# Kernel optimization log

Hardware: AMD Instinct MI355X
Metric: run time of the kernel (lower is better)

The kernel has to match this reference:

```python
import jax, jax.numpy as jnp
import numpy as np

N = 50000
E = 800000
IN_DIM, HID, OUT, DW = 128, 96, 40, 64
N_LBL = 10


def _deg_inv_sqrt(dst, n):
    # PyG gcn_norm: degree over target nodes of (A + I)
    deg = jax.ops.segment_sum(jnp.ones((dst.shape[0],), jnp.float32), dst, num_segments=n) + 1.0
    return jnp.where(deg > 0, 1.0 / jnp.sqrt(deg), 0.0)


def gcn_conv(h_in, W, b, src, dst, dinv):
    # GCNConv: out = D^-1/2 (A + I) D^-1/2 (X W) + b
    h = h_in @ W                                  # [N, F]
    norm = (dinv[src] * dinv[dst])[:, None]       # [E, 1]
    agg = jax.ops.segment_sum(h[src] * norm, dst, num_segments=h.shape[0])
    agg = agg + h * (dinv * dinv)[:, None]        # self-loop term
    return agg + b


def setup_inputs() -> dict:
    key = jax.random.key(0)
    ks = jax.random.split(key, 12)
    inp = {
        "x": jax.random.normal(ks[0], (N, IN_DIM), jnp.float32),
        "y": jax.random.uniform(ks[1], (N, OUT), jnp.float32),
        "edge_index": jax.random.randint(ks[2], (2, E), 0, N, jnp.int64 if jax.config.read("jax_enable_x64") else jnp.int32),
        "deep_walk_emb": jax.random.normal(ks[3], (N, DW), jnp.float32),
        # learned params
        "W_gcn1": jax.random.normal(ks[4], (IN_DIM, HID), jnp.float32) * (1.0 / np.sqrt(IN_DIM)),
        "b_gcn1": jnp.zeros((HID,), jnp.float32),
        "W_gcn2": jax.random.normal(ks[5], (HID, HID), jnp.float32) * (1.0 / np.sqrt(HID)),
        "b_gcn2": jnp.zeros((HID,), jnp.float32),
        "W_lbl": jax.random.normal(ks[6], (N_LBL, OUT, OUT), jnp.float32) * (1.0 / np.sqrt(OUT)),
        "b_lbl": jnp.zeros((N_LBL, OUT), jnp.float32),
        "W_fuse": jax.random.normal(ks[7], (HID + OUT + DW, OUT), jnp.float32) * (1.0 / np.sqrt(HID + OUT + DW)),
        "b_fuse": jnp.zeros((OUT,), jnp.float32),
    }
    return inp


def reference(x, y, edge_index, deep_walk_emb,
              W_gcn1, b_gcn1, W_gcn2, b_gcn2,
              W_lbl, b_lbl, W_fuse, b_fuse):
    src, dst = edge_index[0], edge_index[1]
    dinv = _deg_inv_sqrt(dst, x.shape[0])

    # feature propagation: 2 stacked GCNConv layers
    h = gcn_conv(x, W_gcn1, b_gcn1, src, dst, dinv)
    h = gcn_conv(h, W_gcn2, b_gcn2, src, dst, dinv)

    # label propagation: 10 stacked GCNConv layers via scan over stacked weights
    def step(carry, wb):
        W, b = wb
        return gcn_conv(carry, W, b, src, dst, dinv), None

    x_label, _ = jax.lax.scan(step, y, (W_lbl, b_lbl))

    fused = jnp.concatenate([h, x_label, deep_walk_emb], axis=1)  # [N, HID+OUT+DW]
    out = fused @ W_fuse + b_fuse
    return jax.nn.sigmoid(out)
```

## Files before the change

### kernel.cpp

```cpp
#include <hip/hip_runtime.h>
#include <hip/hip_bf16.h>
#include <math.h>

#define THREADS 256
typedef _Float16 h16;

__device__ __forceinline__ void ld8h(const h16* p, float* f) {
    union { uint4 u; h16 h[8]; } c;
    c.u = *(const uint4*)p;
#pragma unroll
    for (int j = 0; j < 8; ++j) f[j] = (float)c.h[j];
}

__global__ void count_kernel(const int* __restrict__ dst, int* __restrict__ cnt, int E) {
    int e = blockIdx.x * blockDim.x + threadIdx.x;
    if (e < E) atomicAdd(&cnt[dst[e]], 1);
}

__global__ __launch_bounds__(256) void scanp1_pre_kernel(
    const int* __restrict__ cnt, int* __restrict__ partial, int n, int NB,
    const float* __restrict__ Wl, const float* __restrict__ bl,
    const float* __restrict__ W1, const float* __restrict__ W2,
    const float* __restrict__ b1,
    float* __restrict__ C0, float* __restrict__ betas,
    float* __restrict__ W12, float* __restrict__ betaf1)
{
    __shared__ __align__(16) float smem[9216];
    const int tid = threadIdx.x;
    const int bid = blockIdx.x;

    if (bid < NB) {
        int* red = (int*)smem;
        int base = bid * 1024 + tid * 4;
        int s = 0;
        if (base + 3 < n) {
            int4 v = *(const int4*)(cnt + base);
            s = v.x + v.y + v.z + v.w;
        } else {
            for (int k = 0; k < 4; k++) { int i = base + k; if (i < n) s += cnt[i]; }
        }
        red[tid] = s;
        __syncthreads();
        for (int off = 128; off > 0; off >>= 1) {
            if (tid < off) red[tid] += red[tid + off];
            __syncthreads();
        }
        if (tid == 0) partial[bid] = red[0];
        return;
    }

    if (bid == NB) {
        float* Ca  = smem;
        float* Cb  = smem + 1600;
        float* sWm = smem + 3200;
        float* bls = smem + 4800;
        for (int idx = tid; idx < 100; idx += 256)
            ((float4*)bls)[idx] = ((const float4*)bl)[idx];
        for (int idx = tid; idx < 1600; idx += 256)
            Ca[idx] = ((idx / 40) == (idx % 40)) ? 1.f : 0.f;
        if (tid < 40) betas[9 * 40 + tid] = bl[9 * 40 + tid];
        __syncthreads();
        float* cur = Ca;
        float* nxt = Cb;
        for (int m = 9; m >= 0; --m) {
            for (int idx = tid; idx < 400; idx += 256)
                ((float4*)sWm)[idx] = ((const float4*)(Wl + (size_t)m * 1600))[idx];
            __syncthreads();
            for (int sid = tid; sid < 400; sid += 256) {
                int i = sid / 10, jq = sid - (sid / 10) * 10;
                const float* wr = &sWm[i * 40];
                const float4* c4 = (const float4*)cur;
                float4 a = make_float4(0.f, 0.f, 0.f, 0.f);
#pragma unroll
                for (int k = 0; k < 40; ++k) {
                    float w = wr[k];
                    float4 c = c4[k * 10 + jq];
                    a.x = fmaf(w, c.x, a.x); a.y = fmaf(w, c.y, a.y);
                    a.z = fmaf(w, c.z, a.z); a.w = fmaf(w, c.w, a.w);
                }
                ((float4*)nxt)[sid] = a;
            }
            __syncthreads();
            if (m >= 1 && tid < 40) {
                float s = 0.f;
                const float* br = &bls[(m - 1) * 40];
#pragma unroll
                for (int k = 0; k < 40; ++k) s = fmaf(br[k], nxt[k * 40 + tid], s);
                betas[(size_t)(m - 1) * 40 + tid] = s;
            }
            float* t = cur; cur = nxt; nxt = t;
            __syncthreads();
        }
        for (int idx = tid; idx < 1600; idx += 256) C0[idx] = cur[idx];
        return;
    }

    float* sW2 = smem;
    for (int idx = tid; idx < 2304; idx += 256)
        ((float4*)sW2)[idx] = ((const float4*)W2)[idx];
    __syncthreads();
    int idx = (bid - NB - 1) * 256 + tid;
    {
        int i = idx / 96, j = idx - (idx / 96) * 96;
        float s = 0.f;
        const float* wr = W1 + (size_t)i * 96;
#pragma unroll 8
        for (int k = 0; k < 96; ++k) s = fmaf(wr[k], sW2[k * 96 + j], s);
        W12[idx] = s;
    }
    if (bid == NB + 1 && tid < 96) {
        float s = 0.f;
        for (int k = 0; k < 96; ++k) s = fmaf(b1[k], sW2[k * 96 + tid], s);
        betaf1[tid] = s;
    }
}

__global__ __launch_bounds__(256) void scan_p2(int* __restrict__ partial, int* __restrict__ rowptr, int nb, int n) {
    __shared__ int sm[256];
    int tid = threadIdx.x;
    int v = (tid < nb) ? partial[tid] : 0;
    sm[tid] = v;
    __syncthreads();
    int acc = v;
    for (int off = 1; off < 256; off <<= 1) {
        int t = (tid >= off) ? sm[tid - off] : 0;
        __syncthreads();
        acc += t;
        sm[tid] = acc;
        __syncthreads();
    }
    if (tid < nb) partial[tid] = acc - v;
    if (tid == 255) rowptr[n] = sm[255];
}

__global__ __launch_bounds__(256) void scan_p3(const int* __restrict__ cnt, const int* __restrict__ partial,
                                               int* __restrict__ rowptr, int* __restrict__ cursor,
                                               float* __restrict__ dinv, int n) {
    __shared__ int tsum[256];
    int tid = threadIdx.x;
    int base = blockIdx.x * 1024 + tid * 4;
    int v0 = 0, v1 = 0, v2 = 0, v3 = 0;
    if (base + 3 < n) {
        int4 t = *(const int4*)(cnt + base);
        v0 = t.x; v1 = t.y; v2 = t.z; v3 = t.w;
    } else {
        if (base + 0 < n) v0 = cnt[base + 0];
        if (base + 1 < n) v1 = cnt[base + 1];
        if (base + 2 < n) v2 = cnt[base + 2];
        if (base + 3 < n) v3 = cnt[base + 3];
    }
    int s = v0 + v1 + v2 + v3;
    tsum[tid] = s;
    __syncthreads();
    int acc = s;
    for (int off = 1; off < 256; off <<= 1) {
        int t = (tid >= off) ? tsum[tid - off] : 0;
        __syncthreads();
        acc += t;
        tsum[tid] = acc;
        __syncthreads();
    }
    int run = partial[blockIdx.x] + acc - s;
    int vv[4] = {v0, v1, v2, v3};
    for (int k = 0; k < 4; k++) {
        int i = base + k;
        if (i < n) {
            rowptr[i] = run; cursor[i] = run; run += vv[k];
            dinv[i] = rsqrtf((float)vv[k] + 1.0f);
        }
    }
}

template<int FIN, int FOUT, typename TX>
__device__ __forceinline__ void gemm_body(
    const TX* __restrict__ X, const float* __restrict__ W,
    const float* __restrict__ dinv, h16* __restrict__ Y, int n,
    float* sX, float* sW, int bid, int tid)
{
    constexpr int KC = (FIN % 32 == 0) ? 32 : FIN;
    constexpr int NCHUNK = FIN / KC;
    constexpr int TN = (FOUT + 15) / 16;
    constexpr int BM = 64;
    constexpr int KP = KC + 4;

    const int tj = tid & 15;
    const int ti = tid >> 4;
    const int i0 = bid * BM;

    float acc[4][TN] = {};

    for (int c = 0; c < NCHUNK; ++c) {
        const int k0 = c * KC;
        __syncthreads();
        if constexpr (sizeof(TX) == 2) {
            constexpr int K8 = KC / 8;
            for (int v = tid; v < BM * K8; v += 256) {
                int r = v / K8, q = v - r * K8;
                int gi = i0 + r;
                float f[8] = {0.f, 0.f, 0.f, 0.f, 0.f, 0.f, 0.f, 0.f};
                if (gi < n) ld8h((const h16*)X + (size_t)gi * FIN + k0 + q * 8, f);
                float* p = &sX[r * KP + q * 8];
#pragma unroll
                for (int j = 0; j < 8; ++j) p[j] = f[j];
            }
        } else {
            constexpr int K4 = KC / 4;
            for (int v = tid; v < BM * K4; v += 256) {
                int r = v / K4, q = v - r * K4;
                int gi = i0 + r;
                float4 val = (gi < n) ? *(const float4*)((const float*)X + (size_t)gi * FIN + k0 + q * 4)
                                      : make_float4(0.f, 0.f, 0.f, 0.f);
                float* p = &sX[r * KP + q * 4];
                p[0] = val.x; p[1] = val.y; p[2] = val.z; p[3] = val.w;
            }
        }
        for (int v = tid; v < KC * FOUT; v += 256) {
            int kk = v / FOUT;
            int j = v - kk * FOUT;
            sW[j * KP + kk] = W[(size_t)(k0 + kk) * FOUT + j];
        }
        __syncthreads();
#pragma unroll
        for (int kk = 0; kk < KC; kk += 4) {
            float4 xv[4];
#pragma unroll
            for (int m = 0; m < 4; ++m)
                xv[m] = *(const float4*)&sX[(ti + 16 * m) * KP + kk];
#pragma unroll
            for (int u = 0; u < TN; ++u) {
                float4 wv = *(const float4*)&sW[(tj + 16 * u) * KP + kk];
#pragma unroll
                for (int m = 0; m < 4; ++m) {
                    acc[m][u] = fmaf(xv[m].x, wv.x, acc[m][u]);
                    acc[m][u] = fmaf(xv[m].y, wv.y, acc[m][u]);
                    acc[m][u] = fmaf(xv[m].z, wv.z, acc[m][u]);
                    acc[m][u] = fmaf(xv[m].w, wv.w, acc[m][u]);
                }
            }
        }
    }

#pragma unroll
    for (int m = 0; m < 4; ++m) {
        int gi = i0 + ti + 16 * m;
        if (gi >= n) continue;
        float dv = dinv[gi];
#pragma unroll
        for (int u = 0; u < TN; ++u) {
            int j = tj + 16 * u;
            if (j < FOUT) Y[(size_t)gi * FOUT + j] = (h16)(acc[m][u] * dv);
        }
    }
}

template<int FIN, int FOUT, typename TX>
__global__ __launch_bounds__(256) void gemm_kernel(
    const TX* __restrict__ X, const float* __restrict__ W,
    const float* __restrict__ dinv, h16* __restrict__ Y, int n)
{
    constexpr int KC = (FIN % 32 == 0) ? 32 : FIN;
    constexpr int KP = KC + 4;
    constexpr int TN = (FOUT + 15) / 16;
    __shared__ __align__(16) float smem[64 * KP + TN * 16 * KP];
    gemm_body<FIN, FOUT, TX>(X, W, dinv, Y, n, smem, smem + 64 * KP, blockIdx.x, threadIdx.x);
}

__global__ __launch_bounds__(256) void scatter_gemm96_kernel(
    const int* __restrict__ src, const int* __restrict__ dst,
    int* __restrict__ cursor, int* __restrict__ col, int E, int gbE,
    const float* __restrict__ x, const float* __restrict__ W12,
    const float* __restrict__ dinv, h16* __restrict__ A96, int n)
{
    __shared__ __align__(16) float smem[64 * 36 + 96 * 36];
    if (blockIdx.x < gbE) {
        int e = blockIdx.x * 256 + threadIdx.x;
        if (e < E) {
            int d = dst[e];
            int p = atomicAdd(&cursor[d], 1);
            col[p] = src[e];
        }
        return;
    }
    gemm_body<128, 96, float>(x, W12, dinv, A96, n, smem, smem + 64 * 36,
                              blockIdx.x - gbE, threadIdx.x);
}

template<int F, int PRE>
__device__ __forceinline__ void agg_body(
    const h16* __restrict__ hs, const int* __restrict__ rowptr,
    const int* __restrict__ col, const float* __restrict__ dinv,
    const float* __restrict__ bias, h16* __restrict__ out, int n,
    int bid, int tid)
{
    constexpr int F8 = F / 8;
    int gt = bid * 256 + tid;
    if (gt >= n * F8) return;
    int i = gt / F8;
    int f = gt - i * F8;
    int s = rowptr[i], e = rowptr[i + 1];
    const h16* base = hs + (size_t)f * 8;
    float acc[8];
    ld8h(hs + (size_t)i * F + f * 8, acc);
    int k = s;
    for (; k + 8 <= e; k += 8) {
        int c[8];
        union { uint4 u; h16 h[8]; } a[8];
#pragma unroll
        for (int q = 0; q < 8; ++q) c[q] = col[k + q];
#pragma unroll
        for (int q = 0; q < 8; ++q) a[q].u = *(const uint4*)(base + (size_t)c[q] * F);
#pragma unroll
        for (int j = 0; j < 8; ++j) {
            float t0 = ((float)a[0].h[j] + (float)a[1].h[j]) + ((float)a[2].h[j] + (float)a[3].h[j]);
            float t1 = ((float)a[4].h[j] + (float)a[5].h[j]) + ((float)a[6].h[j] + (float)a[7].h[j]);
            acc[j] += t0 + t1;
        }
    }
    for (; k + 4 <= e; k += 4) {
        int c0 = col[k], c1 = col[k + 1], c2 = col[k + 2], c3 = col[k + 3];
        union { uint4 u; h16 h[8]; } a0, a1, a2, a3;
        a0.u = *(const uint4*)(base + (size_t)c0 * F);
        a1.u = *(const uint4*)(base + (size_t)c1 * F);
        a2.u = *(const uint4*)(base + (size_t)c2 * F);
        a3.u = *(const uint4*)(base + (size_t)c3 * F);
#pragma unroll
        for (int j = 0; j < 8; ++j)
            acc[j] += ((float)a0.h[j] + (float)a1.h[j]) + ((float)a2.h[j] + (float)a3.h[j]);
    }
    for (; k < e; k++) {
        float v[8];
        ld8h(base + (size_t)col[k] * F, v);
#pragma unroll
        for (int j = 0; j < 8; ++j) acc[j] += v[j];
    }
    float dv = dinv[i];
    float sc = PRE ? dv : 1.f;
    union { uint4 u; h16 h[8]; } o;
#pragma unroll
    for (int j = 0; j < 8; ++j) o.h[j] = (h16)((acc[j] * dv + bias[f * 8 + j]) * sc);
    *(uint4*)(out + (size_t)i * F + f * 8) = o.u;
}

template<int F, int PRE>
__global__ __launch_bounds__(256) void agg_h(
    const h16* __restrict__ hs, const int* __restrict__ rowptr,
    const int* __restrict__ col, const float* __restrict__ dinv,
    const float* __restrict__ bias, h16* __restrict__ out, int n) {
    agg_body<F, PRE>(hs, rowptr, col, dinv, bias, out, n, blockIdx.x, threadIdx.x);
}

template<int PRE2>
__global__ __launch_bounds__(256) void agg_dual_kernel(
    const h16* __restrict__ hsA, const float* __restrict__ biasA, h16* __restrict__ outA,
    const h16* __restrict__ hsB, const float* __restrict__ biasB, h16* __restrict__ outB,
    const int* __restrict__ rowptr, const int* __restrict__ col,
    const float* __restrict__ dinv, int n, int nblkA)
{
    if (blockIdx.x < nblkA)
        agg_body<40, 1>(hsA, rowptr, col, dinv, biasA, outA, n, blockIdx.x, threadIdx.x);
    else
        agg_body<96, PRE2>(hsB, rowptr, col, dinv, biasB, outB, n, blockIdx.x - nblkA, threadIdx.x);
}

template<int KC, typename T>
__device__ __forceinline__ void fuse_chunk(
    const T* __restrict__ src, int FIN, int k0, int wrow0,
    const float* __restrict__ Wf, float* sX, float* sW,
    float acc[4][3], int i0, int n, int tid)
{
    constexpr int KP = 44;
    __syncthreads();
    if constexpr (sizeof(T) == 2) {
        constexpr int K8 = KC / 8;
        for (int v = tid; v < 64 * K8; v += 256) {
            int r = v / K8, q = v - r * K8;
            int gi = i0 + r;
            float f[8] = {0.f, 0.f, 0.f, 0.f, 0.f, 0.f, 0.f, 0.f};
            if (gi < n) ld8h((const h16*)src + (size_t)gi * FIN + k0 + q * 8, f);
            float* p = &sX[r * KP + q * 8];
#pragma unroll
            for (int j = 0; j < 8; ++j) p[j] = f[j];
        }
    } else {
        constexpr int K4 = KC / 4;
        for (int v = tid; v < 64 * K4; v += 256) {
            int r = v / K4, q = v - r * K4;
            int gi = i0 + r;
            float4 val = (gi < n) ? *(const float4*)((const float*)src + (size_t)gi * FIN + k0 + q * 4)
                                  : make_float4(0.f, 0.f, 0.f, 0.f);
            float* p = &sX[r * KP + q * 4];
            p[0] = val.x; p[1] = val.y; p[2] = val.z; p[3] = val.w;
        }
    }
    for (int v = tid; v < KC * 40; v += 256) {
        int kk = v / 40, j = v - kk * 40;
        sW[j * KP + kk] = Wf[(size_t)(wrow0 + kk) * 40 + j];
    }
    __syncthreads();
    int tj = tid & 15, ti = tid >> 4;
#pragma unroll
    for (int kk = 0; kk < KC; kk += 4) {
        float4 xv[4];
#pragma unroll
        for (int m = 0; m < 4; ++m)
            xv[m] = *(const float4*)&sX[(ti + 16 * m) * KP + kk];
#pragma unroll
        for (int u = 0; u < 3; ++u) {
            float4 wv = *(const float4*)&sW[(tj + 16 * u) * KP + kk];
#pragma unroll
            for (int m = 0; m < 4; ++m) {
                acc[m][u] = fmaf(xv[m].x, wv.x, acc[m][u]);
                acc[m][u] = fmaf(xv[m].y, wv.y, acc[m][u]);
                acc[m][u] = fmaf(xv[m].z, wv.z, acc[m][u]);
                acc[m][u] = fmaf(xv[m].w, wv.w, acc[m][u]);
            }
        }
    }
}

__global__ __launch_bounds__(256) void fuse_gemm_kernel(
    const h16* __restrict__ h2, const h16* __restrict__ xl,
    const float* __restrict__ dw, const float* __restrict__ Wf,
    const float* __restrict__ bf, float* __restrict__ out, int n)
{
    __shared__ __align__(16) float sX[64 * 44];
    __shared__ __align__(16) float sW[48 * 44];
    float acc[4][3] = {};
    const int tid = threadIdx.x;
    const int i0 = blockIdx.x * 64;
    fuse_chunk<32>(h2, 96, 0,  0,   Wf, sX, sW, acc, i0, n, tid);
    fuse_chunk<32>(h2, 96, 32, 32,  Wf, sX, sW, acc, i0, n, tid);
    fuse_chunk<32>(h2, 96, 64, 64,  Wf, sX, sW, acc, i0, n, tid);
    fuse_chunk<40>(xl, 40, 0,  96,  Wf, sX, sW, acc, i0, n, tid);
    fuse_chunk<32>(dw, 64, 0,  136, Wf, sX, sW, acc, i0, n, tid);
    fuse_chunk<32>(dw, 64, 32, 168, Wf, sX, sW, acc, i0, n, tid);
    const int tj = tid & 15, ti = tid >> 4;
#pragma unroll
    for (int m = 0; m < 4; ++m) {
        int gi = i0 + ti + 16 * m;
        if (gi >= n) continue;
#pragma unroll
        for (int u = 0; u < 3; ++u) {
            int j = tj + 16 * u;
            if (j < 40) {
                float t = acc[m][u] + bf[j];
                out[(size_t)gi * 40 + j] = 1.f / (1.f + expf(-t));
            }
        }
    }
}

extern "C" void kernel_launch(void* const* d_in, const int* in_sizes, int n_in,
                              void* d_out, int out_size, void* d_ws, size_t ws_size,
                              hipStream_t stream) {
    const float* x   = (const float*)d_in[0];
    const float* y   = (const float*)d_in[1];
    const int*   ei  = (const int*)d_in[2];
    const float* dwe = (const float*)d_in[3];
    const float* W1  = (const float*)d_in[4];
    const float* b1  = (const float*)d_in[5];
    const float* W2  = (const float*)d_in[6];
    const float* b2  = (const float*)d_in[7];
    const float* Wl  = (const float*)d_in[8];
    const float* bl  = (const float*)d_in[9];
    const float* Wf  = (const float*)d_in[10];
    const float* bf  = (const float*)d_in[11];
    float* out = (float*)d_out;

    const int n = in_sizes[0] / 128;
    const int E = in_sizes[2] / 2;
    const int* srcp = ei;
    const int* dstp = ei + E;

    char* ws = (char*)d_ws;
    size_t off = 0;
    auto alloc = [&](size_t bytes) -> void* {
        void* p = ws + off;
        off += bytes;
        off = (off + 255) & ~(size_t)255;
        return p;
    };

    int*   cnt     = (int*)alloc((size_t)n * 4);
    float* dinv    = (float*)alloc((size_t)n * 4);
    int*   rowptr  = (int*)alloc((size_t)(n + 1) * 4);
    int*   cursor  = (int*)alloc((size_t)n * 4);
    int*   partial = (int*)alloc(256 * 4);
    int*   col     = (int*)alloc((size_t)E * 4);
    h16*   A96     = (h16*)alloc((size_t)n * 96 * 2);
    h16*   B96     = (h16*)alloc((size_t)n * 96 * 2);
    h16*   Z0      = (h16*)alloc((size_t)n * 40 * 2);
    h16*   LA      = (h16*)alloc((size_t)n * 40 * 2);
    h16*   LB      = (h16*)alloc((size_t)n * 40 * 2);
    float* C0      = (float*)alloc(1600 * 4);
    float* betas   = (float*)alloc(10 * 40 * 4);
    float* W12     = (float*)alloc(128 * 96 * 4);
    float* betaf1  = (float*)alloc(96 * 4);
    (void)ws_size;

    const int gb_e    = (E + THREADS - 1) / THREADS;
    const int NB      = (n + 1023) / 1024;
    const int gb_gm   = (n + 63) / 64;
    const int gb_a96  = (n * 12 + THREADS - 1) / THREADS;
    const int gb_a40  = (n * 5 + THREADS - 1) / THREADS;

    hipMemsetAsync(cnt, 0, (size_t)n * 4, stream);
    count_kernel<<<gb_e, THREADS, 0, stream>>>(dstp, cnt, E);
    scanp1_pre_kernel<<<NB + 49, THREADS, 0, stream>>>(
        cnt, partial, n, NB, Wl, bl, W1, W2, b1, C0, betas, W12, betaf1);
    scan_p2<<<1, THREADS, 0, stream>>>(partial, rowptr, NB, n);
    scan_p3<<<NB, THREADS, 0, stream>>>(cnt, partial, rowptr, cursor, dinv, n);

    gemm_kernel<40, 40, float><<<gb_gm, THREADS, 0, stream>>>(y, C0, dinv, Z0, n);

    scatter_gemm96_kernel<<<gb_e + gb_gm, THREADS, 0, stream>>>(
        srcp, dstp, cursor, col, E, gb_e, x, W12, dinv, A96, n);

    agg_dual_kernel<1><<<gb_a40 + gb_a96, THREADS, 0, stream>>>(
        Z0, betas + 0, LA, A96, betaf1, B96, rowptr, col, dinv, n, gb_a40);
    agg_dual_kernel<0><<<gb_a40 + gb_a96, THREADS, 0, stream>>>(
        LA, betas + 40, LB, B96, b2, A96, rowptr, col, dinv, n, gb_a40);

    const h16* cur = LB;
    const h16* xl = LB;
    for (int m = 3; m <= 10; m++) {
        h16* nxt = (m & 1) ? LA : LB;
        if (m < 10)
            agg_h<40, 1><<<gb_a40, THREADS, 0, stream>>>(cur, rowptr, col, dinv, betas + (size_t)(m - 1) * 40, nxt, n);
        else
            agg_h<40, 0><<<gb_a40, THREADS, 0, stream>>>(cur, rowptr, col, dinv, betas + (size_t)(m - 1) * 40, nxt, n);
        cur = nxt;
        xl = nxt;
    }

    fuse_gemm_kernel<<<gb_gm, THREADS, 0, stream>>>(A96, xl, dwe, Wf, bf, out, n);
}
```

Measured before the change: 397.2 us.

## Partition edge counting and CSR scatter by destination range across block classes

Replaces the one-thread-per-edge count and scatter kernels with grid-strided kernels in which each of 8 block classes handles only the destinations in its slice of the node range. Each block therefore issues atomics to a narrower region of memory, which is meant to improve atomic locality in L2. The scatter is also split off from the fused scatter+GEMM kernel into its own launch, and the 128→96 GEMM now runs as a separate kernel. In exchange, every block class reads the full dst array (eight passes over the edges), and an extra kernel launch is added.

```diff
diff --git a/kernel.cpp b/kernel.cpp
--- a/kernel.cpp
+++ b/kernel.cpp
@@ -12,9 +12,38 @@
     for (int j = 0; j < 8; ++j) f[j] = (float)c.h[j];
 }
 
-__global__ void count_kernel(const int* __restrict__ dst, int* __restrict__ cnt, int E) {
-    int e = blockIdx.x * blockDim.x + threadIdx.x;
-    if (e < E) atomicAdd(&cnt[dst[e]], 1);
+__global__ __launch_bounds__(256) void count_part_kernel(
+    const int* __restrict__ dst, int* __restrict__ cnt, int E, int n)
+{
+    const int cls = blockIdx.x & 7;
+    const int nb  = gridDim.x >> 3;
+    const int sub = blockIdx.x >> 3;
+    const int lo = (int)((long long)n * cls / 8);
+    const int hi = (int)((long long)n * (cls + 1) / 8);
+    const int stride = nb * 256;
+    for (int e = sub * 256 + threadIdx.x; e < E; e += stride) {
+        int d = dst[e];
+        if (d >= lo && d < hi) atomicAdd(&cnt[d], 1);
+    }
+}
+
+__global__ __launch_bounds__(256) void scatter_part_kernel(
+    const int* __restrict__ src, const int* __restrict__ dst,
+    int* __restrict__ cursor, int* __restrict__ col, int E, int n)
+{
+    const int cls = blockIdx.x & 7;
+    const int nb  = gridDim.x >> 3;
+    const int sub = blockIdx.x >> 3;
+    const int lo = (int)((long long)n * cls / 8);
+    const int hi = (int)((long long)n * (cls + 1) / 8);
+    const int stride = nb * 256;
+    for (int e = sub * 256 + threadIdx.x; e < E; e += stride) {
+        int d = dst[e];
+        if (d >= lo && d < hi) {
+            int p = atomicAdd(&cursor[d], 1);
+            col[p] = src[e];
+        }
+    }
 }
 
 __global__ __launch_bounds__(256) void scanp1_pre_kernel(
@@ -263,26 +292,6 @@
     constexpr int TN = (FOUT + 15) / 16;
     __shared__ __align__(16) float smem[64 * KP + TN * 16 * KP];
     gemm_body<FIN, FOUT, TX>(X, W, dinv, Y, n, smem, smem + 64 * KP, blockIdx.x, threadIdx.x);
-}
-
-__global__ __launch_bounds__(256) void scatter_gemm96_kernel(
-    const int* __restrict__ src, const int* __restrict__ dst,
-    int* __restrict__ cursor, int* __restrict__ col, int E, int gbE,
-    const float* __restrict__ x, const float* __restrict__ W12,
-    const float* __restrict__ dinv, h16* __restrict__ A96, int n)
-{
-    __shared__ __align__(16) float smem[64 * 36 + 96 * 36];
-    if (blockIdx.x < gbE) {
-        int e = blockIdx.x * 256 + threadIdx.x;
-        if (e < E) {
-            int d = dst[e];
-            int p = atomicAdd(&cursor[d], 1);
-            col[p] = src[e];
-        }
-        return;
-    }
-    gemm_body<128, 96, float>(x, W12, dinv, A96, n, smem, smem + 64 * 36,
-                              blockIdx.x - gbE, threadIdx.x);
 }
 
 template<int F, int PRE>
@@ -498,23 +507,22 @@
     float* betaf1  = (float*)alloc(96 * 4);
     (void)ws_size;
 
-    const int gb_e    = (E + THREADS - 1) / THREADS;
     const int NB      = (n + 1023) / 1024;
     const int gb_gm   = (n + 63) / 64;
     const int gb_a96  = (n * 12 + THREADS - 1) / THREADS;
     const int gb_a40  = (n * 5 + THREADS - 1) / THREADS;
+    const int PART_BLOCKS = 2048;
 
     hipMemsetAsync(cnt, 0, (size_t)n * 4, stream);
-    count_kernel<<<gb_e, THREADS, 0, stream>>>(dstp, cnt, E);
+    count_part_kernel<<<PART_BLOCKS, THREADS, 0, stream>>>(dstp, cnt, E, n);
     scanp1_pre_kernel<<<NB + 49, THREADS, 0, stream>>>(
         cnt, partial, n, NB, Wl, bl, W1, W2, b1, C0, betas, W12, betaf1);
     scan_p2<<<1, THREADS, 0, stream>>>(partial, rowptr, NB, n);
     scan_p3<<<NB, THREADS, 0, stream>>>(cnt, partial, rowptr, cursor, dinv, n);
+    scatter_part_kernel<<<PART_BLOCKS, THREADS, 0, stream>>>(srcp, dstp, cursor, col, E, n);
 
     gemm_kernel<40, 40, float><<<gb_gm, THREADS, 0, stream>>>(y, C0, dinv, Z0, n);
-
-    scatter_gemm96_kernel<<<gb_e + gb_gm, THREADS, 0, stream>>>(
-        srcp, dstp, cursor, col, E, gb_e, x, W12, dinv, A96, n);
+    gemm_kernel<128, 96, float><<<gb_gm, THREADS, 0, stream>>>(x, W12, dinv, A96, n);
 
     agg_dual_kernel<1><<<gb_a40 + gb_a96, THREADS, 0, stream>>>(
         Z0, betas + 0, LA, A96, betaf1, B96, rowptr, col, dinv, n, gb_a40);
```

After: 386.5 us, median of 2. -2.7%, faster.
